# Kernel optimization log

Measured on AMD Instinct MI355X. Metric: run time of the kernel, lower is better.

Reference implementation:

```python
import jax, jax.numpy as jnp
import numpy as np

MARGIN = 0.8  # TripletMarginMiner(margin=0.8, type_of_triplets='semihard')
Z_DIM = 512
N_CONCEPT = 64
NUM_TASK, NUM_SHOT, NUM_WAY = 16, 5, 5


def _triplet_indices(num_shot, num_way):
    # labels = torch.arange(num_way).repeat(num_shot) -> tile pattern
    labels = np.tile(np.arange(num_way), num_shot)
    N = labels.shape[0]
    same = labels[:, None] == labels[None, :]
    pos = same & ~np.eye(N, dtype=bool)          # a != p, same label
    neg = ~same                                  # different label
    a, p, n = np.nonzero(pos[:, :, None] & neg[:, None, :])  # all candidate triplets
    return jnp.asarray(a), jnp.asarray(p), jnp.asarray(n)


def setup_inputs() -> dict:
    key = jax.random.key(0)
    ks = jax.random.split(key, 12)
    d = Z_DIM
    s = lambda fan: 1.0 / np.sqrt(fan)
    inp = {
        'input_data': jax.random.normal(ks[0], (NUM_TASK, NUM_SHOT, NUM_WAY, d), jnp.float32),
        # proj_inner: Linear(3d -> 2d), ReLU, Linear(2d -> d)
        'W1': jax.random.normal(ks[1], (3 * d, 2 * d), jnp.float32) * s(3 * d),
        'b1': jnp.zeros((2 * d,), jnp.float32),
        'W2': jax.random.normal(ks[2], (2 * d, d), jnp.float32) * s(2 * d),
        'b2': jnp.zeros((d,), jnp.float32),
        # proj_outer: Linear(d -> 2d), ReLU, Linear(2d -> d)
        'W3': jax.random.normal(ks[3], (d, 2 * d), jnp.float32) * s(d),
        'b3': jnp.zeros((2 * d,), jnp.float32),
        'W4': jax.random.normal(ks[4], (2 * d, d), jnp.float32) * s(2 * d),
        'b4': jnp.zeros((d,), jnp.float32),
        # cls: Linear(d -> n_concept)
        'Wc': jax.random.normal(ks[5], (d, N_CONCEPT), jnp.float32) * s(d),
        'bc': jnp.zeros((N_CONCEPT,), jnp.float32),
    }
    return inp


def reference(input_data, W1, b1, W2, b2, W3, b3, W4, b4, Wc, bc):
    num_task, num_shot, num_way, d = input_data.shape
    x = input_data.reshape(num_task, num_shot * num_way, d)  # [K, N, d]
    a, p, n = _triplet_indices(num_shot, num_way)            # fixed triplet set [T]

    # --- semihard mining (no grad; binary mask so no grad path anyway) ---
    # LpDistance default: normalize embeddings, then L2 distance
    xn = x / jnp.linalg.norm(x, axis=-1, keepdims=True)
    sq = jnp.sum(xn * xn, axis=-1)                           # [K, N]
    D2 = sq[:, :, None] + sq[:, None, :] - 2.0 * jnp.einsum('kid,kjd->kij', xn, xn)
    D = jnp.sqrt(jnp.clip(D2, 0.0))                          # [K, N, N]
    tm = D[:, a, n] - D[:, a, p]                             # an_dist - ap_dist, [K, T]
    mask = ((tm > 0.0) & (tm <= MARGIN)).astype(x.dtype)     # semihard: 0 < margin <= 0.8

    # --- gather triplet embeddings (unnormalized), concat [x_a, x_p, x_n] ---
    feat = jnp.concatenate([x[:, a], x[:, p], x[:, n]], axis=-1)  # [K, T, 3d]

    # proj_inner then masked sum over mined triplets per task
    h = jax.nn.relu(feat @ W1 + b1) @ W2 + b2                # [K, T, d]
    pooled = jnp.einsum('ktd,kt->kd', h, mask)               # [K, d]

    o = jax.nn.relu(pooled @ W3 + b3) @ W4 + b4              # [K, d]
    score = o @ Wc + bc                                      # [K, n_concept]
    return jax.nn.softmax(score, axis=-1)
```

## Files before the change

kernel.cpp:

```cpp
#include <hip/hip_runtime.h>
#include <math.h>

#define NT 16
#define NR 25
#define DZ 512
#define D2Z 1024
#define NC 64

typedef short bf16x8 __attribute__((ext_vector_type(8)));
typedef float f32x4  __attribute__((ext_vector_type(4)));

#define TP  76
#define XSP 520
#define CP  68

static __device__ inline unsigned short f2bf(float v) {
    union { float f; unsigned u; } x; x.f = v;
    unsigned r = x.u + 0x7fffu + ((x.u >> 16) & 1u);
    return (unsigned short)(r >> 16);
}
static __device__ inline float bf2f(unsigned short h) {
    union { float f; unsigned u; } x; x.u = ((unsigned)h) << 16; return x.f;
}

__global__ __launch_bounds__(256) void k_prep(
    const float* __restrict__ x, const float* __restrict__ W1,
    unsigned short* __restrict__ W1h, unsigned short* __restrict__ W1l,
    float* __restrict__ Dm)
{
    __shared__ unsigned short th[64 * TP], tl[64 * TP];
    int vb = blockIdx.x;
    int tid = threadIdx.x;

    if (vb < 384) {
        int r0 = (vb % 24) * 64;
        int j0 = (vb / 24) * 64;
        int c  = r0 >> 9;
        int rb = r0 & 511;

        #pragma unroll
        for (int it = 0; it < 4; it++) {
            int rl = (tid >> 4) + it * 16;
            int jj = (tid & 15) * 4;
            float4 v = *(const float4*)(W1 + (size_t)(r0 + rl) * D2Z + j0 + jj);
            unsigned short h0 = f2bf(v.x), h1 = f2bf(v.y), h2 = f2bf(v.z), h3 = f2bf(v.w);
            th[rl * TP + jj + 0] = h0; tl[rl * TP + jj + 0] = f2bf(v.x - bf2f(h0));
            th[rl * TP + jj + 1] = h1; tl[rl * TP + jj + 1] = f2bf(v.y - bf2f(h1));
            th[rl * TP + jj + 2] = h2; tl[rl * TP + jj + 2] = f2bf(v.z - bf2f(h2));
            th[rl * TP + jj + 3] = h3; tl[rl * TP + jj + 3] = f2bf(v.w - bf2f(h3));
        }
        __syncthreads();

        #pragma unroll
        for (int it = 0; it < 4; it++) {
            int jl = (tid >> 4) + it * 16;
            int r4 = (tid & 15) * 4;
            ushort4 hv = make_ushort4(th[(r4+0)*TP + jl], th[(r4+1)*TP + jl],
                                      th[(r4+2)*TP + jl], th[(r4+3)*TP + jl]);
            ushort4 lv = make_ushort4(tl[(r4+0)*TP + jl], tl[(r4+1)*TP + jl],
                                      tl[(r4+2)*TP + jl], tl[(r4+3)*TP + jl]);
            size_t dst = ((size_t)c * D2Z + j0 + jl) * DZ + rb + r4;
            *(ushort4*)(W1h + dst) = hv;
            *(ushort4*)(W1l + dst) = lv;
        }
    } else {
        int i = vb - 384;
        int k = i & 15, a = i >> 4;
        int lane = tid & 63;
        int w    = tid >> 6;
        const float* xk = x + (size_t)k * NR * DZ;

        const float4* xap = (const float4*)(xk + a * DZ);
        float4 a0 = xap[lane];
        float4 a1 = xap[lane + 64];

        float sa = a0.x*a0.x + a0.y*a0.y + a0.z*a0.z + a0.w*a0.w
                 + a1.x*a1.x + a1.y*a1.y + a1.z*a1.z + a1.w*a1.w;
        #pragma unroll
        for (int off = 32; off; off >>= 1) sa += __shfl_xor(sa, off);
        float inva = 1.0f / sqrtf(sa);
        a0.x *= inva; a0.y *= inva; a0.z *= inva; a0.w *= inva;
        a1.x *= inva; a1.y *= inva; a1.z *= inva; a1.w *= inva;
        float sqa = a0.x*a0.x + a0.y*a0.y + a0.z*a0.z + a0.w*a0.w
                  + a1.x*a1.x + a1.y*a1.y + a1.z*a1.z + a1.w*a1.w;
        #pragma unroll
        for (int off = 32; off; off >>= 1) sqa += __shfl_xor(sqa, off);

        for (int j = w; j < NR; j += 4) {
            const float4* xjp = (const float4*)(xk + j * DZ);
            float4 j0 = xjp[lane];
            float4 j1 = xjp[lane + 64];
            float sj = j0.x*j0.x + j0.y*j0.y + j0.z*j0.z + j0.w*j0.w
                     + j1.x*j1.x + j1.y*j1.y + j1.z*j1.z + j1.w*j1.w;
            #pragma unroll
            for (int off = 32; off; off >>= 1) sj += __shfl_xor(sj, off);
            float invj = 1.0f / sqrtf(sj);
            j0.x *= invj; j0.y *= invj; j0.z *= invj; j0.w *= invj;
            j1.x *= invj; j1.y *= invj; j1.z *= invj; j1.w *= invj;

            float sqj = j0.x*j0.x + j0.y*j0.y + j0.z*j0.z + j0.w*j0.w
                      + j1.x*j1.x + j1.y*j1.y + j1.z*j1.z + j1.w*j1.w;
            float dij = a0.x*j0.x + a0.y*j0.y + a0.z*j0.z + a0.w*j0.w
                      + a1.x*j1.x + a1.y*j1.y + a1.z*j1.z + a1.w*j1.w;
            #pragma unroll
            for (int off = 32; off; off >>= 1) {
                sqj += __shfl_xor(sqj, off);
                dij += __shfl_xor(dij, off);
            }
            float d2 = sqa + sqj - 2.0f * dij;
            float d  = sqrtf(fmaxf(d2, 0.0f));
            if (lane == 0) Dm[((size_t)k * NR + a) * NR + j] = d;
        }
    }
}

__global__ __launch_bounds__(256, 2) void k_fused(
    const float* __restrict__ x,
    const unsigned short* __restrict__ W1h, const unsigned short* __restrict__ W1l,
    const float* __restrict__ b1, const float* __restrict__ Dm,
    float* __restrict__ G)
{
    __shared__ unsigned short xs_h[25 * XSP], xs_l[25 * XSP];
    __shared__ float Ct[75 * CP];
    __shared__ float Dm_s[NR * NR];
    __shared__ float red[4][64];

    int bid = blockIdx.x;
    int k  = bid >> 4;
    int jt = bid & 15;
    int j0 = jt * 64;

    int tid  = threadIdx.x;
    int lane = tid & 63;
    int w    = tid >> 6;
    int q    = lane >> 4;
    int ln16 = lane & 15;

    for (int idx = tid; idx < NR * NR; idx += 256)
        Dm_s[idx] = Dm[(size_t)k * NR * NR + idx];

    for (int g = tid; g < NR * 64; g += 256) {
        int row = g >> 6;
        int c8  = (g & 63) * 8;
        const float* xp = x + ((size_t)k * NR + row) * DZ + c8;
        float4 v0 = *(const float4*)(xp);
        float4 v1 = *(const float4*)(xp + 4);
        unsigned short h;
        ushort4 ha, hb, la, lb;
        h = f2bf(v0.x); ha.x = h; la.x = f2bf(v0.x - bf2f(h));
        h = f2bf(v0.y); ha.y = h; la.y = f2bf(v0.y - bf2f(h));
        h = f2bf(v0.z); ha.z = h; la.z = f2bf(v0.z - bf2f(h));
        h = f2bf(v0.w); ha.w = h; la.w = f2bf(v0.w - bf2f(h));
        h = f2bf(v1.x); hb.x = h; lb.x = f2bf(v1.x - bf2f(h));
        h = f2bf(v1.y); hb.y = h; lb.y = f2bf(v1.y - bf2f(h));
        h = f2bf(v1.z); hb.z = h; lb.z = f2bf(v1.z - bf2f(h));
        h = f2bf(v1.w); hb.w = h; lb.w = f2bf(v1.w - bf2f(h));
        *(ushort4*)&xs_h[row * XSP + c8]     = ha;
        *(ushort4*)&xs_h[row * XSP + c8 + 4] = hb;
        *(ushort4*)&xs_l[row * XSP + c8]     = la;
        *(ushort4*)&xs_l[row * XSP + c8 + 4] = lb;
    }
    __syncthreads();

    int rowA1 = 16 + ln16;
    if (rowA1 > 24) rowA1 = 24;

    const unsigned short* wb_h = W1h + ((size_t)j0 + w * 16 + ln16) * DZ + q * 8;
    const unsigned short* wb_l = W1l + ((size_t)j0 + w * 16 + ln16) * DZ + q * 8;

    for (int c = 0; c < 3; c++) {
        f32x4 acc0 = (f32x4){0.f,0.f,0.f,0.f};
        f32x4 acc1 = (f32x4){0.f,0.f,0.f,0.f};
        const unsigned short* wch = wb_h + (size_t)c * D2Z * DZ;
        const unsigned short* wcl = wb_l + (size_t)c * D2Z * DZ;

        #pragma unroll
        for (int kc = 0; kc < 16; kc++) {
            int kog = kc * 32 + q * 8;
            bf16x8 b_h = *(const bf16x8*)(wch + kc * 32);
            bf16x8 b_l = *(const bf16x8*)(wcl + kc * 32);
            bf16x8 a0h = *(const bf16x8*)&xs_h[ln16 * XSP + kog];
            bf16x8 a0l = *(const bf16x8*)&xs_l[ln16 * XSP + kog];
            bf16x8 a1h = *(const bf16x8*)&xs_h[rowA1 * XSP + kog];
            bf16x8 a1l = *(const bf16x8*)&xs_l[rowA1 * XSP + kog];
            acc0 = __builtin_amdgcn_mfma_f32_16x16x32_bf16(a0h, b_h, acc0, 0, 0, 0);
            acc0 = __builtin_amdgcn_mfma_f32_16x16x32_bf16(a0h, b_l, acc0, 0, 0, 0);
            acc0 = __builtin_amdgcn_mfma_f32_16x16x32_bf16(a0l, b_h, acc0, 0, 0, 0);
            acc1 = __builtin_amdgcn_mfma_f32_16x16x32_bf16(a1h, b_h, acc1, 0, 0, 0);
            acc1 = __builtin_amdgcn_mfma_f32_16x16x32_bf16(a1h, b_l, acc1, 0, 0, 0);
            acc1 = __builtin_amdgcn_mfma_f32_16x16x32_bf16(a1l, b_h, acc1, 0, 0, 0);
        }

        int col = w * 16 + ln16;
        #pragma unroll
        for (int r = 0; r < 4; r++) {
            int r0 = q * 4 + r;
            Ct[(c * 25 + r0) * CP + col] = acc0[r];
            int r1 = 16 + q * 4 + r;
            if (r1 < 25) Ct[(c * 25 + r1) * CP + col] = acc1[r];
        }
    }
    __syncthreads();

    int j = tid & 63;
    int h = tid >> 6;
    float b1v = b1[j0 + j];

    float a2v[NR], a3v[NR];
    #pragma unroll
    for (int i = 0; i < NR; i++) a2v[i] = Ct[(25 + i) * CP + j];
    #pragma unroll
    for (int i = 0; i < NR; i++) a3v[i] = Ct[(50 + i) * CP + j];

    float acc = 0.0f;
    #pragma unroll
    for (int a = 0; a < NR; a++) {
        const int qa = a % 5, mdiv = a / 5;
        int m = h + (h >= mdiv);
        int p = qa + 5 * m;
        float a1  = Ct[a * CP + j];
        float dap = Dm_s[a * NR + p];
        float s = a1 + a2v[p] + b1v;
        #pragma unroll
        for (int ng = 0; ng < 5; ng++) {
            #pragma unroll
            for (int o = 0; o < 4; o++) {
                int n = ng * 5 + o + (o >= qa);
                float tm = Dm_s[a * NR + n] - dap;
                bool sel = (tm > 0.0f) && (tm <= 0.8f);
                float pre = fmaxf(s + a3v[n], 0.0f);
                float msk = sel ? 1.0f : 0.0f;
                acc = fmaf(msk, pre, acc);
            }
        }
    }
    red[h][j] = acc;
    __syncthreads();
    if (tid < 64)
        G[(size_t)k * D2Z + j0 + tid] = red[0][tid] + red[1][tid]
                                      + red[2][tid] + red[3][tid];
}

__global__ __launch_bounds__(256) void k_pooled(const float* __restrict__ G,
                                                const float* __restrict__ Dm,
                                                const float* __restrict__ W2,
                                                const float* __restrict__ b2,
                                                float* __restrict__ pooled)
{
    int bx = blockIdx.x, k = blockIdx.y;
    int tid = threadIdx.x, lane = tid & 63, kc = tid >> 6;
    int col = bx * 64 + lane;

    const float* Dk = Dm + (size_t)k * NR * NR;
    float cntv = 0.0f;
    for (int idx = tid; idx < 2000; idx += 256) {
        int a   = idx / 80;
        int rem = idx - a * 80;
        int mi  = rem / 20;
        int nn  = rem - mi * 20;
        int qa = a % 5, mdiv = a / 5;
        int m = mi + (mi >= mdiv);
        int p = qa + 5 * m;
        int ng = nn >> 2, o = nn & 3;
        int n = ng * 5 + o + (o >= qa);
        float tm = Dk[a * NR + n] - Dk[a * NR + p];
        cntv += ((tm > 0.0f) && (tm <= 0.8f)) ? 1.0f : 0.0f;
    }
    #pragma unroll
    for (int off = 32; off; off >>= 1) cntv += __shfl_xor(cntv, off);

    __shared__ float red[4][64];
    __shared__ float cred[4];
    if (lane == 0) cred[kc] = cntv;

    const float* Gk = G + (size_t)k * D2Z;
    float a0 = 0.f, a1 = 0.f, a2 = 0.f, a3 = 0.f;
    int j0 = kc * 256;
    #pragma unroll 4
    for (int jj = j0; jj < j0 + 256; jj += 4) {
        a0 = fmaf(Gk[jj+0], W2[(size_t)(jj+0) * DZ + col], a0);
        a1 = fmaf(Gk[jj+1], W2[(size_t)(jj+1) * DZ + col], a1);
        a2 = fmaf(Gk[jj+2], W2[(size_t)(jj+2) * DZ + col], a2);
        a3 = fmaf(Gk[jj+3], W2[(size_t)(jj+3) * DZ + col], a3);
    }
    red[kc][lane] = (a0 + a1) + (a2 + a3);
    __syncthreads();
    if (tid < 64) {
        float cnt = cred[0] + cred[1] + cred[2] + cred[3];
        float s = red[0][lane] + red[1][lane] + red[2][lane] + red[3][lane];
        s += cnt * b2[col];
        pooled[(size_t)k * DZ + col] = s;
    }
}

__global__ __launch_bounds__(256) void k_u(const float* __restrict__ pooled,
                                           const float* __restrict__ W3,
                                           const float* __restrict__ b3,
                                           float* __restrict__ u)
{
    int bx = blockIdx.x, k = blockIdx.y;
    int tid = threadIdx.x, lane = tid & 63, kc = tid >> 6;
    int col = bx * 64 + lane;

    const float* Pk = pooled + (size_t)k * DZ;
    float a0 = 0.f, a1 = 0.f, a2 = 0.f, a3 = 0.f;
    int s0 = kc * 128;
    #pragma unroll 4
    for (int s = s0; s < s0 + 128; s += 4) {
        a0 = fmaf(Pk[s+0], W3[(size_t)(s+0) * D2Z + col], a0);
        a1 = fmaf(Pk[s+1], W3[(size_t)(s+1) * D2Z + col], a1);
        a2 = fmaf(Pk[s+2], W3[(size_t)(s+2) * D2Z + col], a2);
        a3 = fmaf(Pk[s+3], W3[(size_t)(s+3) * D2Z + col], a3);
    }
    __shared__ float red[4][64];
    red[kc][lane] = (a0 + a1) + (a2 + a3);
    __syncthreads();
    if (tid < 64) {
        float v = red[0][lane] + red[1][lane] + red[2][lane] + red[3][lane] + b3[col];
        u[(size_t)k * D2Z + col] = fmaxf(v, 0.0f);
    }
}

__global__ __launch_bounds__(256) void k_o(const float* __restrict__ u,
                                           const float* __restrict__ W4,
                                           const float* __restrict__ b4,
                                           float* __restrict__ o)
{
    int bx = blockIdx.x, k = blockIdx.y;
    int tid = threadIdx.x, lane = tid & 63, kc = tid >> 6;
    int col = bx * 64 + lane;

    const float* Uk = u + (size_t)k * D2Z;
    float a0 = 0.f, a1 = 0.f, a2 = 0.f, a3 = 0.f;
    int j0 = kc * 256;
    #pragma unroll 4
    for (int jj = j0; jj < j0 + 256; jj += 4) {
        a0 = fmaf(Uk[jj+0], W4[(size_t)(jj+0) * DZ + col], a0);
        a1 = fmaf(Uk[jj+1], W4[(size_t)(jj+1) * DZ + col], a1);
        a2 = fmaf(Uk[jj+2], W4[(size_t)(jj+2) * DZ + col], a2);
        a3 = fmaf(Uk[jj+3], W4[(size_t)(jj+3) * DZ + col], a3);
    }
    __shared__ float red[4][64];
    red[kc][lane] = (a0 + a1) + (a2 + a3);
    __syncthreads();
    if (tid < 64) {
        o[(size_t)k * DZ + col] = red[0][lane] + red[1][lane] + red[2][lane]
                                + red[3][lane] + b4[col];
    }
}

__global__ __launch_bounds__(256) void k_score(const float* __restrict__ o,
                                               const float* __restrict__ Wc,
                                               const float* __restrict__ bc,
                                               float* __restrict__ out)
{
    int k = blockIdx.x;
    int tid = threadIdx.x, oc = tid & 63, kc = tid >> 6;

    const float* Ok = o + (size_t)k * DZ;
    float a0 = 0.f, a1 = 0.f, a2 = 0.f, a3 = 0.f;
    int r0 = kc * 128;
    #pragma unroll 4
    for (int rr = r0; rr < r0 + 128; rr += 4) {
        a0 = fmaf(Ok[rr+0], Wc[(size_t)(rr+0) * NC + oc], a0);
        a1 = fmaf(Ok[rr+1], Wc[(size_t)(rr+1) * NC + oc], a1);
        a2 = fmaf(Ok[rr+2], Wc[(size_t)(rr+2) * NC + oc], a2);
        a3 = fmaf(Ok[rr+3], Wc[(size_t)(rr+3) * NC + oc], a3);
    }
    __shared__ float red[4][64];
    red[kc][oc] = (a0 + a1) + (a2 + a3);
    __syncthreads();
    if (tid < 64) {
        float sc = bc[tid] + red[0][tid] + red[1][tid] + red[2][tid] + red[3][tid];
        float m = sc;
        #pragma unroll
        for (int off = 32; off; off >>= 1) m = fmaxf(m, __shfl_xor(m, off));
        float e = expf(sc - m);
        float ss = e;
        #pragma unroll
        for (int off = 32; off; off >>= 1) ss += __shfl_xor(ss, off);
        out[k * NC + tid] = e / ss;
    }
}

extern "C" void kernel_launch(void* const* d_in, const int* in_sizes, int n_in,
                              void* d_out, int out_size, void* d_ws, size_t ws_size,
                              hipStream_t stream)
{
    const float* x  = (const float*)d_in[0];
    const float* W1 = (const float*)d_in[1];
    const float* b1 = (const float*)d_in[2];
    const float* W2 = (const float*)d_in[3];
    const float* b2 = (const float*)d_in[4];
    const float* W3 = (const float*)d_in[5];
    const float* b3 = (const float*)d_in[6];
    const float* W4 = (const float*)d_in[7];
    const float* b4 = (const float*)d_in[8];
    const float* Wc = (const float*)d_in[9];
    const float* bc = (const float*)d_in[10];
    float* out = (float*)d_out;

    float* ws     = (float*)d_ws;
    float* Dm     = ws;
    float* G      = ws + 10016;
    float* pooled = ws + 26400;
    float* uu     = pooled + 8192;
    float* oo     = uu + 16384;
    unsigned short* W1h = (unsigned short*)(oo + 8192);
    unsigned short* W1l = W1h + 3 * D2Z * DZ;

    k_prep  <<<784,            256, 0, stream>>>(x, W1, W1h, W1l, Dm);
    k_fused <<<256,            256, 0, stream>>>(x, W1h, W1l, b1, Dm, G);
    k_pooled<<<dim3(8, NT),    256, 0, stream>>>(G, Dm, W2, b2, pooled);
    k_u     <<<dim3(16, NT),   256, 0, stream>>>(pooled, W3, b3, uu);
    k_o     <<<dim3(8, NT),    256, 0, stream>>>(uu, W4, b4, oo);
    k_score <<<NT,             256, 0, stream>>>(oo, Wc, bc, out);
}
```

Before: 150.7 us.

## Fuse MLP tail into one kernel, prefetch tail weights into cache during prep

Replaces the four small tail kernels (pooled, u, o, score) with one per-task kernel of 1024 threads that keeps the intermediates in shared memory. The mined-triplet count moves into the fused kernel's jt==0 blocks. Extra prep blocks read W2/W3/W4/Wc and discard the sums so those weights are warm in L2/LLC before the tail runs. This cuts launch count and round trips of intermediates through global memory, but the tail now runs on only 16 blocks, which may limit bandwidth per task.

```diff
diff --git a/kernel.cpp b/kernel.cpp
--- a/kernel.cpp
+++ b/kernel.cpp
@@ -26,7 +26,9 @@
 __global__ __launch_bounds__(256) void k_prep(
     const float* __restrict__ x, const float* __restrict__ W1,
     unsigned short* __restrict__ W1h, unsigned short* __restrict__ W1l,
-    float* __restrict__ Dm)
+    float* __restrict__ Dm,
+    const float* __restrict__ W2, const float* __restrict__ W3,
+    const float* __restrict__ W4, const float* __restrict__ Wc)
 {
     __shared__ unsigned short th[64 * TP], tl[64 * TP];
     int vb = blockIdx.x;
@@ -63,7 +65,7 @@
             *(ushort4*)(W1h + dst) = hv;
             *(ushort4*)(W1l + dst) = lv;
         }
-    } else {
+    } else if (vb < 784) {
         int i = vb - 384;
         int k = i & 15, a = i >> 4;
         int lane = tid & 63;
@@ -111,6 +113,24 @@
             float d  = sqrtf(fmaxf(d2, 0.0f));
             if (lane == 0) Dm[((size_t)k * NR + a) * NR + j] = d;
         }
+    } else {
+        int pb = vb - 784;
+        float s = 0.0f;
+        #pragma unroll
+        for (int it = 0; it < 7; it++) {
+            int idx = pb * 256 + tid + it * 61440;
+            if (idx < 401408) {
+                const float* base;
+                int off;
+                if (idx < 131072)      { base = W2; off = idx; }
+                else if (idx < 262144) { base = W3; off = idx - 131072; }
+                else if (idx < 393216) { base = W4; off = idx - 262144; }
+                else                   { base = Wc; off = idx - 393216; }
+                float4 v = *((const float4*)base + off);
+                s += v.x + v.y + v.z + v.w;
+            }
+        }
+        asm volatile("" :: "v"(s));
     }
 }
 
@@ -118,12 +138,13 @@
     const float* __restrict__ x,
     const unsigned short* __restrict__ W1h, const unsigned short* __restrict__ W1l,
     const float* __restrict__ b1, const float* __restrict__ Dm,
-    float* __restrict__ G)
+    float* __restrict__ G, float* __restrict__ cnt)
 {
     __shared__ unsigned short xs_h[25 * XSP], xs_l[25 * XSP];
     __shared__ float Ct[75 * CP];
     __shared__ float Dm_s[NR * NR];
     __shared__ float red[4][64];
+    __shared__ float cred[4];
 
     int bid = blockIdx.x;
     int k  = bid >> 4;
@@ -162,6 +183,26 @@
     }
     __syncthreads();
 
+    if (jt == 0) {
+        float cntv = 0.0f;
+        for (int idx = tid; idx < 2000; idx += 256) {
+            int a   = idx / 80;
+            int rem = idx - a * 80;
+            int mi  = rem / 20;
+            int nn  = rem - mi * 20;
+            int qa = a % 5, mdiv = a / 5;
+            int m = mi + (mi >= mdiv);
+            int p = qa + 5 * m;
+            int ng = nn >> 2, o = nn & 3;
+            int n = ng * 5 + o + (o >= qa);
+            float tm = Dm_s[a * NR + n] - Dm_s[a * NR + p];
+            cntv += ((tm > 0.0f) && (tm <= 0.8f)) ? 1.0f : 0.0f;
+        }
+        #pragma unroll
+        for (int off = 32; off; off >>= 1) cntv += __shfl_xor(cntv, off);
+        if (lane == 0) cred[w] = cntv;
+    }
+
     int rowA1 = 16 + ln16;
     if (rowA1 > 24) rowA1 = 24;
 
@@ -202,13 +243,14 @@
     }
     __syncthreads();
 
+    if (jt == 0 && tid == 0)
+        cnt[k] = cred[0] + cred[1] + cred[2] + cred[3];
+
     int j = tid & 63;
     int h = tid >> 6;
     float b1v = b1[j0 + j];
 
-    float a2v[NR], a3v[NR];
-    #pragma unroll
-    for (int i = 0; i < NR; i++) a2v[i] = Ct[(25 + i) * CP + j];
+    float a3v[NR];
     #pragma unroll
     for (int i = 0; i < NR; i++) a3v[i] = Ct[(50 + i) * CP + j];
 
@@ -220,7 +262,7 @@
         int p = qa + 5 * m;
         float a1  = Ct[a * CP + j];
         float dap = Dm_s[a * NR + p];
-        float s = a1 + a2v[p] + b1v;
+        float s = a1 + Ct[(25 + p) * CP + j] + b1v;
         #pragma unroll
         for (int ng = 0; ng < 5; ng++) {
             #pragma unroll
@@ -241,145 +283,87 @@
                                       + red[2][tid] + red[3][tid];
 }
 
-__global__ __launch_bounds__(256) void k_pooled(const float* __restrict__ G,
-                                                const float* __restrict__ Dm,
-                                                const float* __restrict__ W2,
-                                                const float* __restrict__ b2,
-                                                float* __restrict__ pooled)
+__global__ __launch_bounds__(1024) void k_tail(
+    const float* __restrict__ G,  const float* __restrict__ cnt,
+    const float* __restrict__ W2, const float* __restrict__ b2,
+    const float* __restrict__ W3, const float* __restrict__ b3,
+    const float* __restrict__ W4, const float* __restrict__ b4,
+    const float* __restrict__ Wc, const float* __restrict__ bc,
+    float* __restrict__ out)
 {
-    int bx = blockIdx.x, k = blockIdx.y;
-    int tid = threadIdx.x, lane = tid & 63, kc = tid >> 6;
-    int col = bx * 64 + lane;
-
-    const float* Dk = Dm + (size_t)k * NR * NR;
-    float cntv = 0.0f;
-    for (int idx = tid; idx < 2000; idx += 256) {
-        int a   = idx / 80;
-        int rem = idx - a * 80;
-        int mi  = rem / 20;
-        int nn  = rem - mi * 20;
-        int qa = a % 5, mdiv = a / 5;
-        int m = mi + (mi >= mdiv);
-        int p = qa + 5 * m;
-        int ng = nn >> 2, o = nn & 3;
-        int n = ng * 5 + o + (o >= qa);
-        float tm = Dk[a * NR + n] - Dk[a * NR + p];
-        cntv += ((tm > 0.0f) && (tm <= 0.8f)) ? 1.0f : 0.0f;
-    }
-    #pragma unroll
-    for (int off = 32; off; off >>= 1) cntv += __shfl_xor(cntv, off);
-
-    __shared__ float red[4][64];
-    __shared__ float cred[4];
-    if (lane == 0) cred[kc] = cntv;
-
-    const float* Gk = G + (size_t)k * D2Z;
-    float a0 = 0.f, a1 = 0.f, a2 = 0.f, a3 = 0.f;
-    int j0 = kc * 256;
-    #pragma unroll 4
-    for (int jj = j0; jj < j0 + 256; jj += 4) {
-        a0 = fmaf(Gk[jj+0], W2[(size_t)(jj+0) * DZ + col], a0);
-        a1 = fmaf(Gk[jj+1], W2[(size_t)(jj+1) * DZ + col], a1);
-        a2 = fmaf(Gk[jj+2], W2[(size_t)(jj+2) * DZ + col], a2);
-        a3 = fmaf(Gk[jj+3], W2[(size_t)(jj+3) * DZ + col], a3);
-    }
-    red[kc][lane] = (a0 + a1) + (a2 + a3);
+    __shared__ float Gs[D2Z];
+    __shared__ float Ps[DZ];
+    __shared__ float Us[D2Z];
+    __shared__ float Os[DZ];
+    __shared__ float tmp[1024];
+
+    int k = blockIdx.x;
+    int t = threadIdx.x;
+
+    Gs[t] = G[(size_t)k * D2Z + t];
     __syncthreads();
-    if (tid < 64) {
-        float cnt = cred[0] + cred[1] + cred[2] + cred[3];
-        float s = red[0][lane] + red[1][lane] + red[2][lane] + red[3][lane];
-        s += cnt * b2[col];
-        pooled[(size_t)k * DZ + col] = s;
-    }
-}
-
-__global__ __launch_bounds__(256) void k_u(const float* __restrict__ pooled,
-                                           const float* __restrict__ W3,
-                                           const float* __restrict__ b3,
-                                           float* __restrict__ u)
-{
-    int bx = blockIdx.x, k = blockIdx.y;
-    int tid = threadIdx.x, lane = tid & 63, kc = tid >> 6;
-    int col = bx * 64 + lane;
-
-    const float* Pk = pooled + (size_t)k * DZ;
-    float a0 = 0.f, a1 = 0.f, a2 = 0.f, a3 = 0.f;
-    int s0 = kc * 128;
-    #pragma unroll 4
-    for (int s = s0; s < s0 + 128; s += 4) {
-        a0 = fmaf(Pk[s+0], W3[(size_t)(s+0) * D2Z + col], a0);
-        a1 = fmaf(Pk[s+1], W3[(size_t)(s+1) * D2Z + col], a1);
-        a2 = fmaf(Pk[s+2], W3[(size_t)(s+2) * D2Z + col], a2);
-        a3 = fmaf(Pk[s+3], W3[(size_t)(s+3) * D2Z + col], a3);
-    }
-    __shared__ float red[4][64];
-    red[kc][lane] = (a0 + a1) + (a2 + a3);
-    __syncthreads();
-    if (tid < 64) {
-        float v = red[0][lane] + red[1][lane] + red[2][lane] + red[3][lane] + b3[col];
-        u[(size_t)k * D2Z + col] = fmaxf(v, 0.0f);
-    }
-}
-
-__global__ __launch_bounds__(256) void k_o(const float* __restrict__ u,
-                                           const float* __restrict__ W4,
-                                           const float* __restrict__ b4,
-                                           float* __restrict__ o)
-{
-    int bx = blockIdx.x, k = blockIdx.y;
-    int tid = threadIdx.x, lane = tid & 63, kc = tid >> 6;
-    int col = bx * 64 + lane;
-
-    const float* Uk = u + (size_t)k * D2Z;
-    float a0 = 0.f, a1 = 0.f, a2 = 0.f, a3 = 0.f;
-    int j0 = kc * 256;
-    #pragma unroll 4
-    for (int jj = j0; jj < j0 + 256; jj += 4) {
-        a0 = fmaf(Uk[jj+0], W4[(size_t)(jj+0) * DZ + col], a0);
-        a1 = fmaf(Uk[jj+1], W4[(size_t)(jj+1) * DZ + col], a1);
-        a2 = fmaf(Uk[jj+2], W4[(size_t)(jj+2) * DZ + col], a2);
-        a3 = fmaf(Uk[jj+3], W4[(size_t)(jj+3) * DZ + col], a3);
-    }
-    __shared__ float red[4][64];
-    red[kc][lane] = (a0 + a1) + (a2 + a3);
-    __syncthreads();
-    if (tid < 64) {
-        o[(size_t)k * DZ + col] = red[0][lane] + red[1][lane] + red[2][lane]
-                                + red[3][lane] + b4[col];
-    }
-}
-
-__global__ __launch_bounds__(256) void k_score(const float* __restrict__ o,
-                                               const float* __restrict__ Wc,
-                                               const float* __restrict__ bc,
-                                               float* __restrict__ out)
-{
-    int k = blockIdx.x;
-    int tid = threadIdx.x, oc = tid & 63, kc = tid >> 6;
-
-    const float* Ok = o + (size_t)k * DZ;
-    float a0 = 0.f, a1 = 0.f, a2 = 0.f, a3 = 0.f;
-    int r0 = kc * 128;
-    #pragma unroll 4
-    for (int rr = r0; rr < r0 + 128; rr += 4) {
-        a0 = fmaf(Ok[rr+0], Wc[(size_t)(rr+0) * NC + oc], a0);
-        a1 = fmaf(Ok[rr+1], Wc[(size_t)(rr+1) * NC + oc], a1);
-        a2 = fmaf(Ok[rr+2], Wc[(size_t)(rr+2) * NC + oc], a2);
-        a3 = fmaf(Ok[rr+3], Wc[(size_t)(rr+3) * NC + oc], a3);
-    }
-    __shared__ float red[4][64];
-    red[kc][oc] = (a0 + a1) + (a2 + a3);
-    __syncthreads();
-    if (tid < 64) {
-        float sc = bc[tid] + red[0][tid] + red[1][tid] + red[2][tid] + red[3][tid];
-        float m = sc;
-        #pragma unroll
-        for (int off = 32; off; off >>= 1) m = fmaxf(m, __shfl_xor(m, off));
-        float e = expf(sc - m);
-        float ss = e;
-        #pragma unroll
-        for (int off = 32; off; off >>= 1) ss += __shfl_xor(ss, off);
-        out[k * NC + tid] = e / ss;
+
+    {
+        int c = t & 511, hf = t >> 9;
+        const float* Wp = W2 + (size_t)(hf * 512) * DZ + c;
+        const float* Gp = Gs + hf * 512;
+        float acc = 0.0f;
+        #pragma unroll 16
+        for (int jj = 0; jj < 512; jj++)
+            acc = fmaf(Gp[jj], Wp[(size_t)jj * DZ], acc);
+        tmp[t] = acc;
+        __syncthreads();
+        if (t < 512) Ps[t] = tmp[t] + tmp[t + 512] + cnt[k] * b2[t];
+        __syncthreads();
+    }
+
+    {
+        const float* Wp = W3 + t;
+        float acc = 0.0f;
+        #pragma unroll 16
+        for (int c = 0; c < 512; c++)
+            acc = fmaf(Ps[c], Wp[(size_t)c * D2Z], acc);
+        Us[t] = fmaxf(acc + b3[t], 0.0f);
+        __syncthreads();
+    }
+
+    {
+        int c = t & 511, hf = t >> 9;
+        const float* Wp = W4 + (size_t)(hf * 512) * DZ + c;
+        const float* Up = Us + hf * 512;
+        float acc = 0.0f;
+        #pragma unroll 16
+        for (int ss = 0; ss < 512; ss++)
+            acc = fmaf(Up[ss], Wp[(size_t)ss * DZ], acc);
+        tmp[t] = acc;
+        __syncthreads();
+        if (t < 512) Os[t] = tmp[t] + tmp[t + 512] + b4[t];
+        __syncthreads();
+    }
+
+    {
+        int oc = t & 63, seg = t >> 6;
+        const float* Wp = Wc + (size_t)(seg * 32) * NC + oc;
+        const float* Op = Os + seg * 32;
+        float acc = 0.0f;
+        #pragma unroll
+        for (int r = 0; r < 32; r++)
+            acc = fmaf(Op[r], Wp[(size_t)r * NC], acc);
+        tmp[t] = acc;
+        __syncthreads();
+        if (t < 64) {
+            float sc = bc[t];
+            #pragma unroll
+            for (int g2 = 0; g2 < 16; g2++) sc += tmp[g2 * 64 + t];
+            float m = sc;
+            #pragma unroll
+            for (int off = 32; off; off >>= 1) m = fmaxf(m, __shfl_xor(m, off));
+            float e = expf(sc - m);
+            float ssum = e;
+            #pragma unroll
+            for (int off = 32; off; off >>= 1) ssum += __shfl_xor(ssum, off);
+            out[k * NC + t] = e / ssum;
+        }
     }
 }
 
@@ -400,19 +384,14 @@
     const float* bc = (const float*)d_in[10];
     float* out = (float*)d_out;
 
-    float* ws     = (float*)d_ws;
-    float* Dm     = ws;
-    float* G      = ws + 10016;
-    float* pooled = ws + 26400;
-    float* uu     = pooled + 8192;
-    float* oo     = uu + 16384;
-    unsigned short* W1h = (unsigned short*)(oo + 8192);
+    float* ws   = (float*)d_ws;
+    float* Dm   = ws;
+    float* cnt  = ws + 10016;
+    float* G    = ws + 10032;
+    unsigned short* W1h = (unsigned short*)(ws + 26416);
     unsigned short* W1l = W1h + 3 * D2Z * DZ;
 
-    k_prep  <<<784,            256, 0, stream>>>(x, W1, W1h, W1l, Dm);
-    k_fused <<<256,            256, 0, stream>>>(x, W1h, W1l, b1, Dm, G);
-    k_pooled<<<dim3(8, NT),    256, 0, stream>>>(G, Dm, W2, b2, pooled);
-    k_u     <<<dim3(16, NT),   256, 0, stream>>>(pooled, W3, b3, uu);
-    k_o     <<<dim3(8, NT),    256, 0, stream>>>(uu, W4, b4, oo);
-    k_score <<<NT,             256, 0, stream>>>(oo, Wc, bc, out);
-}
+    k_prep <<<1024, 256, 0, stream>>>(x, W1, W1h, W1l, Dm, W2, W3, W4, Wc);
+    k_fused<<<256,  256, 0, stream>>>(x, W1h, W1l, b1, Dm, G, cnt);
+    k_tail <<<NT,  1024, 0, stream>>>(G, cnt, W2, b2, W3, b3, W4, b4, Wc, bc, out);
+}
```

After: 182.0 us. 20.8% more time.
